# Kernel tuning notes

Measured on AMD Instinct MI355X. Metric: run time of the kernel, lower is better.

## Reference

```python
import jax, jax.numpy as jnp
import numpy as np


def setup_inputs() -> dict:
    key = jax.random.key(0)
    k1, k2, k3, k4 = jax.random.split(key, 4)
    N, E, F_IN, F_OUT = 50000, 800000, 128, 128
    x = jax.random.normal(k1, (N, F_IN), dtype=jnp.float32)
    src = jax.random.randint(k2, (E,), 0, N, dtype=jnp.int32)
    dst = jax.random.randint(k3, (E,), 0, N, dtype=jnp.int32)
    # Linear(2*in, out, bias=False) weight, torch layout (out, 2*in)
    W = jax.random.normal(k4, (F_OUT, 2 * F_IN), dtype=jnp.float32) * (1.0 / np.sqrt(2 * F_IN))
    return {"x": x, "src": src, "dst": dst, "num_nodes": N, "W": W}


def reference(x, src, dst, num_nodes, W):
    # Mean aggregation over sparse adjacency (edge list src -> dst):
    # aggregated[v] = mean_{u in N(v)} x[u]
    msgs = x[src]                                            # [E, F] gather
    summed = jax.ops.segment_sum(msgs, dst, num_segments=num_nodes)  # [N, F]
    deg = jax.ops.segment_sum(jnp.ones_like(dst, dtype=x.dtype), dst,
                              num_segments=num_nodes)        # [N]
    agg = summed / jnp.maximum(deg, 1.0)[:, None]            # mean, safe for isolated nodes
    h = jnp.concatenate([x, agg], axis=1)                    # [N, 2F]
    out = h @ W.T                                            # [N, F_out]
    return jax.nn.relu(out)
```

## Files before the change

kernel.cpp:

```cpp
#include <hip/hip_runtime.h>
#include <hip/hip_bf16.h>

typedef __attribute__((ext_vector_type(8))) short short8;
typedef __attribute__((ext_vector_type(4))) float f32x4;

#define BKS      7
#define BKN      128
#define ITERA    16
#define NBMAX    512
#define CAPB_MAX 5632

__device__ __forceinline__ unsigned short f2bf(float f) {
    unsigned u = __builtin_bit_cast(unsigned, f);
    u += 0x7fffu + ((u >> 16) & 1u);
    return (unsigned short)(u >> 16);
}
__device__ __forceinline__ float bf2f(unsigned short b) {
    return __builtin_bit_cast(float, ((unsigned)b) << 16);
}

__global__ void prep_kernel(const float* __restrict__ x,
                            unsigned short* __restrict__ xb,
                            const float* __restrict__ W,
                            unsigned short* __restrict__ Wp,
                            unsigned* __restrict__ gcur, int nb, int nx8) {
    int i = blockIdx.x * blockDim.x + threadIdx.x;
    if (i < nx8) {
        const float4* p = (const float4*)(x + (size_t)i * 8);
        float4 lo = p[0], hi = p[1];
        short8 v;
        v[0] = (short)f2bf(lo.x); v[1] = (short)f2bf(lo.y);
        v[2] = (short)f2bf(lo.z); v[3] = (short)f2bf(lo.w);
        v[4] = (short)f2bf(hi.x); v[5] = (short)f2bf(hi.y);
        v[6] = (short)f2bf(hi.z); v[7] = (short)f2bf(hi.w);
        *(short8*)(xb + (size_t)i * 8) = v;
    }
    if (i < 4096) {
        const float4* p = (const float4*)(W + (size_t)i * 8);
        float4 lo = p[0], hi = p[1];
        short8 v;
        v[0] = (short)f2bf(lo.x); v[1] = (short)f2bf(lo.y);
        v[2] = (short)f2bf(lo.z); v[3] = (short)f2bf(lo.w);
        v[4] = (short)f2bf(hi.x); v[5] = (short)f2bf(hi.y);
        v[6] = (short)f2bf(hi.z); v[7] = (short)f2bf(hi.w);
        int r    = i >> 5;
        int c0   = (i & 31) << 3;
        int ct   = r >> 4;
        int arow = r & 15;
        int ks   = c0 >> 5;
        int kgrp = (c0 >> 3) & 3;
        int l    = arow | (kgrp << 4);
        *(short8*)(Wp + (((size_t)(ct * 8 + ks) * 64 + l) * 8)) = v;
    }
    if (i < nb) gcur[i] = 0u;
}

__global__ __launch_bounds__(256) void bin_kernel(const int* __restrict__ src,
                                                  const int* __restrict__ dst,
                                                  unsigned* gcur,
                                                  unsigned* __restrict__ gbuf,
                                                  int E, int nb, int capb) {
    __shared__ unsigned cnt[NBMAX];
    __shared__ unsigned gbase[NBMAX];
    for (int t = threadIdx.x; t < nb; t += 256) cnt[t] = 0u;
    __syncthreads();

    int e0 = blockIdx.x * (256 * ITERA) + threadIdx.x;
    unsigned pk[ITERA];
    unsigned short bk[ITERA], pp[ITERA];
#pragma unroll
    for (int it = 0; it < ITERA; ++it) {
        int e = e0 + it * 256;
        bk[it] = 0xFFFFu;
        if (e < E) {
            int d = dst[e];
            unsigned b = (unsigned)d >> BKS;
            pk[it] = (unsigned)src[e] | ((unsigned)(d & (BKN - 1)) << 24);
            pp[it] = (unsigned short)atomicAdd(&cnt[b], 1u);
            bk[it] = (unsigned short)b;
        }
    }
    __syncthreads();
    for (int t = threadIdx.x; t < nb; t += 256)
        gbase[t] = cnt[t] ? atomicAdd(&gcur[t], cnt[t]) : 0u;
    __syncthreads();
#pragma unroll
    for (int it = 0; it < ITERA; ++it) {
        if (bk[it] != 0xFFFFu) {
            unsigned b = bk[it];
            unsigned off = gbase[b] + pp[it];
            if (off < (unsigned)capb) gbuf[(size_t)b * capb + off] = pk[it];
        }
    }
}

__global__ __launch_bounds__(1024) void agg_kernel(const unsigned short* __restrict__ xb,
                                                   const unsigned* __restrict__ gbuf,
                                                   const unsigned* __restrict__ gcur,
                                                   unsigned short* __restrict__ aggb,
                                                   int N, int capb) {
    __shared__ unsigned cnt[BKN];
    __shared__ unsigned degs[BKN];
    __shared__ unsigned cur[BKN];
    __shared__ unsigned elist[CAPB_MAX];

    int tid = threadIdx.x;
    int b   = blockIdx.x;
    unsigned cntB = gcur[b];
    if (cntB > (unsigned)capb) cntB = (unsigned)capb;
    const unsigned* bb = gbuf + (size_t)b * capb;

    if (tid < BKN) cnt[tid] = 0u;
    __syncthreads();
    for (unsigned i = tid; i < cntB; i += 1024)
        atomicAdd(&cnt[bb[i] >> 24], 1u);
    __syncthreads();
    if (tid < BKN) degs[tid] = cnt[tid];
    __syncthreads();
#pragma unroll
    for (int off = 1; off < BKN; off <<= 1) {
        unsigned t = (tid < BKN && tid >= off) ? cnt[tid - off] : 0u;
        __syncthreads();
        if (tid < BKN) cnt[tid] += t;
        __syncthreads();
    }
    if (tid < BKN) cur[tid] = cnt[tid] - degs[tid];
    __syncthreads();
    for (unsigned i = tid; i < cntB; i += 1024) {
        unsigned pk = bb[i];
        unsigned p  = atomicAdd(&cur[pk >> 24], 1u);
        elist[p] = pk & 0x00FFFFFFu;
    }
    __syncthreads();

    int wv = tid >> 6, l = tid & 63;
    int q4 = l >> 4, ql = l & 15;
    int base = b << BKS;

    for (int r0 = wv; r0 < BKN; r0 += 16) {
        unsigned endi  = cnt[r0];
        unsigned dg    = degs[r0];
        unsigned start = endi - dg;
        float acc[8] = {0.f, 0.f, 0.f, 0.f, 0.f, 0.f, 0.f, 0.f};

        unsigned e = start + q4;
        for (; e + 4 < endi; e += 8) {
            unsigned s0 = elist[e];
            unsigned s1 = elist[e + 4];
            short8 v0 = *(const short8*)(xb + (size_t)s0 * 128 + ql * 8);
            short8 v1 = *(const short8*)(xb + (size_t)s1 * 128 + ql * 8);
#pragma unroll
            for (int j = 0; j < 8; ++j)
                acc[j] += bf2f((unsigned short)v0[j]) + bf2f((unsigned short)v1[j]);
        }
        if (e < endi) {
            unsigned s0 = elist[e];
            short8 v0 = *(const short8*)(xb + (size_t)s0 * 128 + ql * 8);
#pragma unroll
            for (int j = 0; j < 8; ++j) acc[j] += bf2f((unsigned short)v0[j]);
        }

#pragma unroll
        for (int j = 0; j < 8; ++j) {
            acc[j] += __shfl_xor(acc[j], 16);
            acc[j] += __shfl_xor(acc[j], 32);
        }
        int node = base + r0;
        if (q4 == 0 && node < N) {
            float inv = dg ? 1.0f / (float)dg : 1.0f;
            short8 st;
#pragma unroll
            for (int j = 0; j < 8; ++j) st[j] = (short)f2bf(acc[j] * inv);
            *(short8*)(aggb + (size_t)node * 128 + ql * 8) = st;
        }
    }
}

__global__ __launch_bounds__(256) void gemm_kernel(const unsigned short* __restrict__ xb,
                                                   const unsigned short* __restrict__ aggb,
                                                   const unsigned short* __restrict__ Wp,
                                                   float* __restrict__ out, int N) {
    int lane = threadIdx.x & 63;
    int wave = threadIdx.x >> 6;
    int v0   = blockIdx.x * 64 + wave * 16;
    int arow = lane & 15;
    int kgrp = lane >> 4;
    int row  = v0 + arow;
    bool rok = row < N;

    short8 afrag[8];
#pragma unroll
    for (int ks = 0; ks < 4; ++ks) {
        short8 a = {};
        if (rok) a = *(const short8*)(xb + (size_t)row * 128 + ks * 32 + kgrp * 8);
        afrag[ks] = a;
    }
#pragma unroll
    for (int ks = 0; ks < 4; ++ks) {
        short8 a = {};
        if (rok) a = *(const short8*)(aggb + (size_t)row * 128 + ks * 32 + kgrp * 8);
        afrag[4 + ks] = a;
    }

    f32x4 acc[8];
#pragma unroll
    for (int ct = 0; ct < 8; ++ct) acc[ct] = (f32x4){0.f, 0.f, 0.f, 0.f};

#pragma unroll
    for (int ks = 0; ks < 8; ++ks) {
        short8 a = afrag[ks];
#pragma unroll
        for (int ct = 0; ct < 8; ++ct) {
            const short8* bp =
                (const short8*)(Wp + (((size_t)(ct * 8 + ks) * 64 + lane) * 8));
            acc[ct] = __builtin_amdgcn_mfma_f32_16x16x32_bf16(a, *bp, acc[ct], 0, 0, 0);
        }
    }

#pragma unroll
    for (int ct = 0; ct < 8; ++ct) {
#pragma unroll
        for (int r = 0; r < 4; ++r) {
            int orow = v0 + kgrp * 4 + r;
            if (orow < N) {
                out[(size_t)orow * 128 + ct * 16 + arow] = fmaxf(acc[ct][r], 0.0f);
            }
        }
    }
}

extern "C" void kernel_launch(void* const* d_in, const int* in_sizes, int n_in,
                              void* d_out, int out_size, void* d_ws, size_t ws_size,
                              hipStream_t stream) {
    const float* x  = (const float*)d_in[0];
    const int* src  = (const int*)d_in[1];
    const int* dst  = (const int*)d_in[2];
    const float* W  = (const float*)d_in[4];

    int N = in_sizes[0] / 128;
    int E = in_sizes[1];
    float* out = (float*)d_out;

    int nb = (N + BKN - 1) >> BKS;
    int capb = 2 * (E / (nb > 0 ? nb : 1)) + 1024;
    capb = (capb + 63) & ~63;
    if (capb > CAPB_MAX) capb = CAPB_MAX;

    char* ws = (char*)d_ws;
    size_t o = 0;
    auto carve = [&](size_t bytes) {
        char* p = ws + o;
        o += (bytes + 255) & ~(size_t)255;
        return p;
    };
    unsigned* gcur       = (unsigned*)carve((size_t)nb * 4);
    unsigned* gbuf       = (unsigned*)carve((size_t)nb * capb * 4);
    unsigned short* Wp   = (unsigned short*)carve(128 * 256 * 2);
    unsigned short* xb   = (unsigned short*)carve((size_t)N * 128 * 2);
    unsigned short* aggb = (unsigned short*)carve((size_t)N * 128 * 2);
    (void)ws_size;

    int nx8 = N * 16;
    int pt  = nx8 > 4096 ? nx8 : 4096;
    if (pt < nb) pt = nb;

    prep_kernel<<<(pt + 255) / 256, 256, 0, stream>>>(x, xb, W, Wp, gcur, nb, nx8);
    bin_kernel<<<(E + 256 * ITERA - 1) / (256 * ITERA), 256, 0, stream>>>(
        src, dst, gcur, gbuf, E, nb, capb);
    agg_kernel<<<nb, 1024, 0, stream>>>(xb, gbuf, gcur, aggb, N, capb);
    gemm_kernel<<<(N + 63) / 64, 256, 0, stream>>>(xb, aggb, Wp, out, N);
}
```

Baseline: 80.70 us.

## Fuse mean aggregation and GEMM into one kernel via shared-memory staging

The aggregation kernel now writes each bucket's 128 mean-aggregated rows into a padded LDS tile instead of global memory. After a barrier, the same 1024-thread block runs the MFMA GEMM: 16 waves split the bucket into 8 row tiles by 2 column halves. This removes the aggb global round trip and one kernel launch. In exchange, LDS use per block grows (about 34KB), and the GEMM now runs at one block per bucket, 391 blocks of 1024 threads, which may lower occupancy and overlap.

```diff
diff --git a/kernel.cpp b/kernel.cpp
--- a/kernel.cpp
+++ b/kernel.cpp
@@ -94,15 +94,18 @@
     }
 }
 
-__global__ __launch_bounds__(1024) void agg_kernel(const unsigned short* __restrict__ xb,
-                                                   const unsigned* __restrict__ gbuf,
-                                                   const unsigned* __restrict__ gcur,
-                                                   unsigned short* __restrict__ aggb,
-                                                   int N, int capb) {
+__global__ __launch_bounds__(1024) void agg_gemm_kernel(
+    const unsigned short* __restrict__ xb,
+    const unsigned* __restrict__ gbuf,
+    const unsigned* __restrict__ gcur,
+    const unsigned short* __restrict__ Wp,
+    float* __restrict__ out, int N, int capb)
+{
     __shared__ unsigned cnt[BKN];
     __shared__ unsigned degs[BKN];
     __shared__ unsigned cur[BKN];
     __shared__ unsigned elist[CAPB_MAX];
+    __shared__ unsigned short aggs[BKN][136];
 
     int tid = threadIdx.x;
     int b   = blockIdx.x;
@@ -165,27 +168,22 @@
             acc[j] += __shfl_xor(acc[j], 16);
             acc[j] += __shfl_xor(acc[j], 32);
         }
-        int node = base + r0;
-        if (q4 == 0 && node < N) {
+        if (q4 == 0) {
             float inv = dg ? 1.0f / (float)dg : 1.0f;
             short8 st;
 #pragma unroll
             for (int j = 0; j < 8; ++j) st[j] = (short)f2bf(acc[j] * inv);
-            *(short8*)(aggb + (size_t)node * 128 + ql * 8) = st;
-        }
-    }
-}
-
-__global__ __launch_bounds__(256) void gemm_kernel(const unsigned short* __restrict__ xb,
-                                                   const unsigned short* __restrict__ aggb,
-                                                   const unsigned short* __restrict__ Wp,
-                                                   float* __restrict__ out, int N) {
-    int lane = threadIdx.x & 63;
-    int wave = threadIdx.x >> 6;
-    int v0   = blockIdx.x * 64 + wave * 16;
-    int arow = lane & 15;
-    int kgrp = lane >> 4;
-    int row  = v0 + arow;
+            *(short8*)&aggs[r0][ql * 8] = st;
+        }
+    }
+    __syncthreads();
+
+    int w    = tid >> 6;
+    int rt   = w >> 1;
+    int cth  = w & 1;
+    int arow = l & 15;
+    int kgrp = l >> 4;
+    int row  = base + rt * 16 + arow;
     bool rok = row < N;
 
     short8 afrag[8];
@@ -196,34 +194,33 @@
         afrag[ks] = a;
     }
 #pragma unroll
-    for (int ks = 0; ks < 4; ++ks) {
-        short8 a = {};
-        if (rok) a = *(const short8*)(aggb + (size_t)row * 128 + ks * 32 + kgrp * 8);
-        afrag[4 + ks] = a;
-    }
-
-    f32x4 acc[8];
-#pragma unroll
-    for (int ct = 0; ct < 8; ++ct) acc[ct] = (f32x4){0.f, 0.f, 0.f, 0.f};
+    for (int ks = 0; ks < 4; ++ks)
+        afrag[4 + ks] = *(const short8*)&aggs[rt * 16 + arow][ks * 32 + kgrp * 8];
+
+    f32x4 acc[4];
+#pragma unroll
+    for (int c = 0; c < 4; ++c) acc[c] = (f32x4){0.f, 0.f, 0.f, 0.f};
 
 #pragma unroll
     for (int ks = 0; ks < 8; ++ks) {
         short8 a = afrag[ks];
 #pragma unroll
-        for (int ct = 0; ct < 8; ++ct) {
+        for (int c = 0; c < 4; ++c) {
+            int ct = cth * 4 + c;
             const short8* bp =
-                (const short8*)(Wp + (((size_t)(ct * 8 + ks) * 64 + lane) * 8));
-            acc[ct] = __builtin_amdgcn_mfma_f32_16x16x32_bf16(a, *bp, acc[ct], 0, 0, 0);
-        }
-    }
-
-#pragma unroll
-    for (int ct = 0; ct < 8; ++ct) {
+                (const short8*)(Wp + (((size_t)(ct * 8 + ks) * 64 + l) * 8));
+            acc[c] = __builtin_amdgcn_mfma_f32_16x16x32_bf16(a, *bp, acc[c], 0, 0, 0);
+        }
+    }
+
+#pragma unroll
+    for (int c = 0; c < 4; ++c) {
 #pragma unroll
         for (int r = 0; r < 4; ++r) {
-            int orow = v0 + kgrp * 4 + r;
+            int orow = base + rt * 16 + kgrp * 4 + r;
             if (orow < N) {
-                out[(size_t)orow * 128 + ct * 16 + arow] = fmaxf(acc[ct][r], 0.0f);
+                out[(size_t)orow * 128 + (cth * 4 + c) * 16 + arow] =
+                    fmaxf(acc[c][r], 0.0f);
             }
         }
     }
@@ -253,11 +250,10 @@
         o += (bytes + 255) & ~(size_t)255;
         return p;
     };
-    unsigned* gcur       = (unsigned*)carve((size_t)nb * 4);
-    unsigned* gbuf       = (unsigned*)carve((size_t)nb * capb * 4);
-    unsigned short* Wp   = (unsigned short*)carve(128 * 256 * 2);
-    unsigned short* xb   = (unsigned short*)carve((size_t)N * 128 * 2);
-    unsigned short* aggb = (unsigned short*)carve((size_t)N * 128 * 2);
+    unsigned* gcur     = (unsigned*)carve((size_t)nb * 4);
+    unsigned* gbuf     = (unsigned*)carve((size_t)nb * capb * 4);
+    unsigned short* Wp = (unsigned short*)carve(128 * 256 * 2);
+    unsigned short* xb = (unsigned short*)carve((size_t)N * 128 * 2);
     (void)ws_size;
 
     int nx8 = N * 16;
@@ -267,6 +263,5 @@
     prep_kernel<<<(pt + 255) / 256, 256, 0, stream>>>(x, xb, W, Wp, gcur, nb, nx8);
     bin_kernel<<<(E + 256 * ITERA - 1) / (256 * ITERA), 256, 0, stream>>>(
         src, dst, gcur, gbuf, E, nb, capb);
-    agg_kernel<<<nb, 1024, 0, stream>>>(xb, gbuf, gcur, aggb, N, capb);
-    gemm_kernel<<<(N + 63) / 64, 256, 0, stream>>>(xb, aggb, Wp, out, N);
-}
+    agg_gemm_kernel<<<nb, 1024, 0, stream>>>(xb, gbuf, gcur, Wp, out, N, capb);
+}
```

New measurement: 79.23 us. Within noise of the previous version (-1.8%).
